# Kernel optimization log

Measured on AMD Instinct MI355X. Metric: run time of the kernel, lower is better.

The kernel has to match this reference:

```python
import jax, jax.numpy as jnp
import numpy as np

EPS = 1e-5
N_GROUP = 1

def _linear(x, w, b):
    # w: [in, out], b: [out]
    return x @ w + b

def _group_norm_per_sample(x, weight, bias, n_group=N_GROUP, eps=EPS):
    # x: [B, C]; weight/bias: [B, C] (per-sample hypernet-generated affine).
    # F.group_norm on 2D input normalizes each sample over its channel groups.
    B, C = x.shape
    xr = x.reshape(B, n_group, C // n_group)
    m = jnp.mean(xr, axis=-1, keepdims=True)
    v = jnp.mean((xr - m) ** 2, axis=-1, keepdims=True)
    xn = ((xr - m) * jax.lax.rsqrt(v + eps)).reshape(B, C)
    return xn * weight + bias

def setup_inputs() -> dict:
    key = jax.random.key(0)
    ks = jax.random.split(key, 32)
    B, P, CIN, COUT = 32768, 8, 512, 256
    s = 0.05
    d = {}
    d['x_feature'] = jax.random.normal(ks[0], (B, CIN), dtype=jnp.float32)
    d['x_param'] = jax.random.normal(ks[1], (B, P), dtype=jnp.float32)
    # hypernet for norm1 weight/bias (P -> 32 -> 2048)
    d['hw1_1_w'] = jax.random.normal(ks[2], (P, 32)) * s;   d['hw1_1_b'] = jnp.zeros((32,))
    d['hw1_2_w'] = jax.random.normal(ks[3], (32, 2048)) * s; d['hw1_2_b'] = jnp.ones((2048,))
    d['hb1_1_w'] = jax.random.normal(ks[4], (P, 32)) * s;   d['hb1_1_b'] = jnp.zeros((32,))
    d['hb1_2_w'] = jax.random.normal(ks[5], (32, 2048)) * s; d['hb1_2_b'] = jnp.zeros((2048,))
    # hypernet for norm2 weight/bias (P -> 32 -> 1024)
    d['hw2_1_w'] = jax.random.normal(ks[6], (P, 32)) * s;   d['hw2_1_b'] = jnp.zeros((32,))
    d['hw2_2_w'] = jax.random.normal(ks[7], (32, 1024)) * s; d['hw2_2_b'] = jnp.ones((1024,))
    d['hb2_1_w'] = jax.random.normal(ks[8], (P, 32)) * s;   d['hb2_1_b'] = jnp.zeros((32,))
    d['hb2_2_w'] = jax.random.normal(ks[9], (32, 1024)) * s; d['hb2_2_b'] = jnp.zeros((1024,))
    # base net
    d['l1_w'] = jax.random.normal(ks[10], (CIN, 2048)) * s;  d['l1_b'] = jnp.zeros((2048,))
    d['l2_w'] = jax.random.normal(ks[11], (2048, 1024)) * s; d['l2_b'] = jnp.zeros((1024,))
    d['l3_w'] = jax.random.normal(ks[12], (1024, COUT)) * s; d['l3_b'] = jnp.zeros((COUT,))
    return d

def reference(x_feature, x_param,
              hw1_1_w, hw1_1_b, hw1_2_w, hw1_2_b,
              hb1_1_w, hb1_1_b, hb1_2_w, hb1_2_b,
              hw2_1_w, hw2_1_b, hw2_2_w, hw2_2_b,
              hb2_1_w, hb2_1_b, hb2_2_w, hb2_2_b,
              l1_w, l1_b, l2_w, l2_b, l3_w, l3_b):
    # hypernet: per-sample group-norm affine params
    p = x_param  # already n_level columns
    w1 = _linear(jax.nn.relu(_linear(p, hw1_1_w, hw1_1_b)), hw1_2_w, hw1_2_b)  # [B, 2048]
    b1 = _linear(jax.nn.relu(_linear(p, hb1_1_w, hb1_1_b)), hb1_2_w, hb1_2_b)  # [B, 2048]
    w2 = _linear(jax.nn.relu(_linear(p, hw2_1_w, hw2_1_b)), hw2_2_w, hw2_2_b)  # [B, 1024]
    b2 = _linear(jax.nn.relu(_linear(p, hb2_1_w, hb2_1_b)), hb2_2_w, hb2_2_b)  # [B, 1024]
    # base net with per-sample affine group norm (vectorized form of the torch
    # host-side grouping loop: samples with identical x_param share identical
    # generated affine params, and group_norm stats are per-sample anyway)
    x = _linear(x_feature, l1_w, l1_b)            # [B, 2048]
    x = jax.nn.relu(_group_norm_per_sample(x, w1, b1))
    x = _linear(x, l2_w, l2_b)                    # [B, 1024]
    x = jax.nn.relu(_group_norm_per_sample(x, w2, b2))
    x = _linear(x, l3_w, l3_b)                    # [B, 256]
    return jax.nn.log_softmax(x, axis=1)
```

## Files before the change

kernel.cpp:

```cpp
#include <hip/hip_runtime.h>

typedef unsigned short u16;
typedef float f32x4 __attribute__((ext_vector_type(4)));
typedef __bf16 bf16x8 __attribute__((ext_vector_type(8)));
typedef u16 u16x4 __attribute__((ext_vector_type(4)));
typedef u16 u16x8 __attribute__((ext_vector_type(8)));

__device__ __forceinline__ float bf2f(u16 u) {
    unsigned int x = ((unsigned int)u) << 16;
    return __builtin_bit_cast(float, x);
}
__device__ __forceinline__ u16 f2bf(float f) {
    unsigned int x = __builtin_bit_cast(unsigned int, f);
    x += 0x7fffu + ((x >> 16) & 1u);
    return (u16)(x >> 16);
}

#define GLD16(gp, lp)                                                          \
    __builtin_amdgcn_global_load_lds(                                          \
        (const __attribute__((address_space(1))) void*)(gp),                   \
        (__attribute__((address_space(3))) void*)(lp), 16, 0, 0)

__global__ void f32_to_bf16_k(const float* __restrict__ in, u16* __restrict__ out, long n4) {
    long i = (long)blockIdx.x * 256 + threadIdx.x;
    if (i >= n4) return;
    f32x4 v = *reinterpret_cast<const f32x4*>(in + i * 4);
    u16x4 o;
    o[0] = f2bf(v[0]); o[1] = f2bf(v[1]); o[2] = f2bf(v[2]); o[3] = f2bf(v[3]);
    *reinterpret_cast<u16x4*>(out + i * 4) = o;
}

__global__ void transpose_f32_bf16(const float* __restrict__ in, u16* __restrict__ out,
                                   int R, int C) {
    __shared__ float tile[32][33];
    const int bx = blockIdx.x * 32;
    const int by = blockIdx.y * 32;
    const int tx = threadIdx.x;
    const int ty0 = threadIdx.y;
    #pragma unroll
    for (int ty = ty0; ty < 32; ty += 8)
        tile[ty][tx] = in[(long)(by + ty) * C + bx + tx];
    __syncthreads();
    #pragma unroll
    for (int ty = ty0; ty < 32; ty += 8)
        out[(long)(bx + ty) * R + by + tx] = f2bf(tile[tx][ty]);
}

__global__ void hyper_h(const float* __restrict__ P, const float* __restrict__ W,
                        const float* __restrict__ b, u16* __restrict__ H, int B_) {
    const int idx = blockIdx.x * 256 + threadIdx.x;
    const int s = idx >> 5, c = idx & 31;
    if (s >= B_) return;
    float acc = b[c];
    #pragma unroll
    for (int k = 0; k < 8; ++k) acc += P[s * 8 + k] * W[k * 32 + c];
    H[idx] = f2bf(fmaxf(acc, 0.f));
}

template <int OUT_BF16>
__global__ __launch_bounds__(256, 2) void gemm_bt(
    const u16* __restrict__ A, const u16* __restrict__ BT,
    const float* __restrict__ bias, u16* __restrict__ Cb, float* __restrict__ Cf,
    int M, int N, int K) {
    __shared__ __align__(16) u16 As[128 * 64];
    __shared__ __align__(16) u16 Bs[128 * 64];
    const int tid = threadIdx.x;
    const int lane = tid & 63;
    const int wave = tid >> 6;
    const int wr = wave >> 1, wc = wave & 1;
    const long row0 = (long)blockIdx.x * 128;
    const long col0 = (long)blockIdx.y * 128;

    const int srow = tid >> 3;
    const int scol = (tid & 7) * 8;
    const u16* Ag = A + (row0 + srow) * (long)K + scol;
    const u16* Bg = BT + (col0 + srow) * (long)K + scol;
    u16* AsW = As + (size_t)(wave * 64) * 8;
    u16* BsW = Bs + (size_t)(wave * 64) * 8;

    f32x4 acc[4][4] = {};

    for (int k0 = 0; k0 < K; k0 += 64) {
        #pragma unroll
        for (int i = 0; i < 4; ++i) {
            GLD16(Ag + (long)i * 32 * K + k0, AsW + i * 256 * 8);
            GLD16(Bg + (long)i * 32 * K + k0, BsW + i * 256 * 8);
        }
        __syncthreads();
        #pragma unroll
        for (int kk = 0; kk < 2; ++kk) {
            bf16x8 af[4], bfr[4];
            #pragma unroll
            for (int m = 0; m < 4; ++m)
                af[m] = *reinterpret_cast<const bf16x8*>(
                    As + (wr * 64 + m * 16 + (lane & 15)) * 64 + kk * 32 + (lane >> 4) * 8);
            #pragma unroll
            for (int n = 0; n < 4; ++n)
                bfr[n] = *reinterpret_cast<const bf16x8*>(
                    Bs + (wc * 64 + n * 16 + (lane & 15)) * 64 + kk * 32 + (lane >> 4) * 8);
            #pragma unroll
            for (int m = 0; m < 4; ++m)
                #pragma unroll
                for (int n = 0; n < 4; ++n)
                    acc[m][n] = __builtin_amdgcn_mfma_f32_16x16x32_bf16(af[m], bfr[n],
                                                                        acc[m][n], 0, 0, 0);
        }
        __syncthreads();
    }

    #pragma unroll
    for (int n = 0; n < 4; ++n) {
        const long col = col0 + wc * 64 + n * 16 + (lane & 15);
        const float bv = bias[col];
        #pragma unroll
        for (int m = 0; m < 4; ++m) {
            const long rowb = row0 + wr * 64 + m * 16 + ((lane >> 4) * 4);
            #pragma unroll
            for (int r = 0; r < 4; ++r) {
                const float v = acc[m][n][r] + bv;
                if (OUT_BF16) Cb[(rowb + r) * (long)N + col] = f2bf(v);
                else          Cf[(rowb + r) * (long)N + col] = v;
            }
        }
    }
}

template <int C>
__global__ __launch_bounds__(256, 2) void gn_affine(
    u16* __restrict__ Y,
    const u16* __restrict__ Hw, const u16* __restrict__ Hb,
    const u16* __restrict__ WwT, const u16* __restrict__ WbT,
    const float* __restrict__ bw, const float* __restrict__ bb) {
    const int tid = threadIdx.x;
    const int lane = tid & 63;
    const int wave = tid >> 6;
    const long r0 = (long)blockIdx.x * 32;
    __shared__ float mean_l[32], rs_l[32];
    __shared__ __align__(16) float wt[32][132];
    __shared__ __align__(16) float btl[32][132];

    const int row = tid >> 3, sub = tid & 7;

    {
        float s = 0.f, ss = 0.f;
        const u16* yr = Y + (r0 + row) * (long)C;
        for (int c = sub * 16; c < C; c += 128) {
            u16x8 v0 = *reinterpret_cast<const u16x8*>(yr + c);
            u16x8 v1 = *reinterpret_cast<const u16x8*>(yr + c + 8);
            #pragma unroll
            for (int j = 0; j < 8; ++j) {
                float f0 = bf2f(v0[j]), f1 = bf2f(v1[j]);
                s += f0 + f1;
                ss += f0 * f0 + f1 * f1;
            }
        }
        s  += __shfl_xor(s, 1);  s  += __shfl_xor(s, 2);  s  += __shfl_xor(s, 4);
        ss += __shfl_xor(ss, 1); ss += __shfl_xor(ss, 2); ss += __shfl_xor(ss, 4);
        if (sub == 0) {
            float m = s / (float)C;
            float var = fmaxf(ss / (float)C - m * m, 0.f);
            mean_l[row] = m;
            rs_l[row] = rsqrtf(var + 1e-5f);
        }
    }
    __syncthreads();

    const int mm = wave & 1;
    const int npair = wave >> 1;
    const bf16x8 ha = *reinterpret_cast<const bf16x8*>(
        Hw + (r0 + mm * 16 + (lane & 15)) * 32 + (lane >> 4) * 8);
    const bf16x8 hbf = *reinterpret_cast<const bf16x8*>(
        Hb + (r0 + mm * 16 + (lane & 15)) * 32 + (lane >> 4) * 8);

    for (int c0 = 0; c0 < C; c0 += 128) {
        #pragma unroll
        for (int j = 0; j < 4; ++j) {
            const int n = npair * 4 + j;
            const int cl = c0 + n * 16 + (lane & 15);
            const bf16x8 wv = *reinterpret_cast<const bf16x8*>(WwT + (long)cl * 32 + (lane >> 4) * 8);
            const bf16x8 bv = *reinterpret_cast<const bf16x8*>(WbT + (long)cl * 32 + (lane >> 4) * 8);
            f32x4 z = {0.f, 0.f, 0.f, 0.f};
            f32x4 wa = __builtin_amdgcn_mfma_f32_16x16x32_bf16(ha, wv, z, 0, 0, 0);
            f32x4 ba = __builtin_amdgcn_mfma_f32_16x16x32_bf16(hbf, bv, z, 0, 0, 0);
            const float bwv = bw[cl], bbv = bb[cl];
            const int ncol = n * 16 + (lane & 15);
            #pragma unroll
            for (int r = 0; r < 4; ++r) {
                const int rl = mm * 16 + (lane >> 4) * 4 + r;
                wt[rl][ncol]  = wa[r] + bwv;
                btl[rl][ncol] = ba[r] + bbv;
            }
        }
        __syncthreads();
        {
            const long base = (r0 + row) * (long)C + c0 + sub * 16;
            u16x8 v0 = *reinterpret_cast<const u16x8*>(Y + base);
            u16x8 v1 = *reinterpret_cast<const u16x8*>(Y + base + 8);
            const float mu = mean_l[row], rs = rs_l[row];
            u16x8 o0, o1;
            #pragma unroll
            for (int j = 0; j < 8; ++j) {
                float f = (bf2f(v0[j]) - mu) * rs;
                f = f * wt[row][sub * 16 + j] + btl[row][sub * 16 + j];
                o0[j] = f2bf(fmaxf(f, 0.f));
                float g = (bf2f(v1[j]) - mu) * rs;
                g = g * wt[row][sub * 16 + 8 + j] + btl[row][sub * 16 + 8 + j];
                o1[j] = f2bf(fmaxf(g, 0.f));
            }
            *reinterpret_cast<u16x8*>(Y + base) = o0;
            *reinterpret_cast<u16x8*>(Y + base + 8) = o1;
        }
        __syncthreads();
    }
}

__global__ __launch_bounds__(256) void logsoftmax256(const float* __restrict__ X,
                                                     float* __restrict__ O) {
    const int wave = threadIdx.x >> 6, lane = threadIdx.x & 63;
    const long row = (long)blockIdx.x * 4 + wave;
    const float* x = X + row * 256 + lane * 4;
    f32x4 v = *reinterpret_cast<const f32x4*>(x);
    float mx = fmaxf(fmaxf(v[0], v[1]), fmaxf(v[2], v[3]));
    #pragma unroll
    for (int d = 1; d < 64; d <<= 1) mx = fmaxf(mx, __shfl_xor(mx, d));
    float s = 0.f;
    #pragma unroll
    for (int j = 0; j < 4; ++j) s += __expf(v[j] - mx);
    #pragma unroll
    for (int d = 1; d < 64; d <<= 1) s += __shfl_xor(s, d);
    const float lse = mx + logf(s);
    f32x4 o;
    #pragma unroll
    for (int j = 0; j < 4; ++j) o[j] = v[j] - lse;
    *reinterpret_cast<f32x4*>(O + row * 256 + lane * 4) = o;
}

extern "C" void kernel_launch(void* const* d_in, const int* in_sizes, int n_in,
                              void* d_out, int out_size, void* d_ws, size_t ws_size,
                              hipStream_t stream) {
    const float* x_feature = (const float*)d_in[0];
    const float* x_param   = (const float*)d_in[1];
    const float* hw1_1_w = (const float*)d_in[2];
    const float* hw1_1_b = (const float*)d_in[3];
    const float* hw1_2_w = (const float*)d_in[4];
    const float* hw1_2_b = (const float*)d_in[5];
    const float* hb1_1_w = (const float*)d_in[6];
    const float* hb1_1_b = (const float*)d_in[7];
    const float* hb1_2_w = (const float*)d_in[8];
    const float* hb1_2_b = (const float*)d_in[9];
    const float* hw2_1_w = (const float*)d_in[10];
    const float* hw2_1_b = (const float*)d_in[11];
    const float* hw2_2_w = (const float*)d_in[12];
    const float* hw2_2_b = (const float*)d_in[13];
    const float* hb2_1_w = (const float*)d_in[14];
    const float* hb2_1_b = (const float*)d_in[15];
    const float* hb2_2_w = (const float*)d_in[16];
    const float* hb2_2_b = (const float*)d_in[17];
    const float* l1_w = (const float*)d_in[18];
    const float* l1_b = (const float*)d_in[19];
    const float* l2_w = (const float*)d_in[20];
    const float* l2_b = (const float*)d_in[21];
    const float* l3_w = (const float*)d_in[22];
    const float* l3_b = (const float*)d_in[23];

    const int B = in_sizes[0] / 512;
    constexpr int CIN = 512, C1 = 2048, C2 = 1024, COUT = 256;

    char* p = (char*)d_ws;
    auto carve = [&](size_t bytes) {
        char* q = p;
        p += (bytes + 255) & ~(size_t)255;
        return q;
    };
    u16* xb    = (u16*)carve((size_t)B * CIN * 2);
    u16* y1    = (u16*)carve((size_t)B * C1 * 2);
    u16* y2    = (u16*)carve((size_t)B * C2 * 2);
    u16* w1T   = (u16*)carve((size_t)C1 * CIN * 2);
    u16* w2T   = (u16*)carve((size_t)C2 * C1 * 2);
    u16* w3T   = (u16*)carve((size_t)COUT * C2 * 2);
    u16* hw12T = (u16*)carve((size_t)C1 * 32 * 2);
    u16* hb12T = (u16*)carve((size_t)C1 * 32 * 2);
    u16* hw22T = (u16*)carve((size_t)C2 * 32 * 2);
    u16* hb22T = (u16*)carve((size_t)C2 * 32 * 2);
    u16* Hw1   = (u16*)carve((size_t)B * 32 * 2);
    u16* Hb1   = (u16*)carve((size_t)B * 32 * 2);
    u16* Hw2   = (u16*)carve((size_t)B * 32 * 2);
    u16* Hb2   = (u16*)carve((size_t)B * 32 * 2);
    float* logits = (float*)y1;

    f32_to_bf16_k<<<(B * CIN / 4 + 255) / 256, 256, 0, stream>>>(x_feature, xb, (long)B * CIN / 4);
    dim3 tb(32, 8);
    transpose_f32_bf16<<<dim3(C1 / 32, CIN / 32), tb, 0, stream>>>(l1_w, w1T, CIN, C1);
    transpose_f32_bf16<<<dim3(C2 / 32, C1 / 32), tb, 0, stream>>>(l2_w, w2T, C1, C2);
    transpose_f32_bf16<<<dim3(COUT / 32, C2 / 32), tb, 0, stream>>>(l3_w, w3T, C2, COUT);
    transpose_f32_bf16<<<dim3(C1 / 32, 1), tb, 0, stream>>>(hw1_2_w, hw12T, 32, C1);
    transpose_f32_bf16<<<dim3(C1 / 32, 1), tb, 0, stream>>>(hb1_2_w, hb12T, 32, C1);
    transpose_f32_bf16<<<dim3(C2 / 32, 1), tb, 0, stream>>>(hw2_2_w, hw22T, 32, C2);
    transpose_f32_bf16<<<dim3(C2 / 32, 1), tb, 0, stream>>>(hb2_2_w, hb22T, 32, C2);
    hyper_h<<<B * 32 / 256, 256, 0, stream>>>(x_param, hw1_1_w, hw1_1_b, Hw1, B);
    hyper_h<<<B * 32 / 256, 256, 0, stream>>>(x_param, hb1_1_w, hb1_1_b, Hb1, B);
    hyper_h<<<B * 32 / 256, 256, 0, stream>>>(x_param, hw2_1_w, hw2_1_b, Hw2, B);
    hyper_h<<<B * 32 / 256, 256, 0, stream>>>(x_param, hb2_1_w, hb2_1_b, Hb2, B);

    gemm_bt<1><<<dim3(B / 128, C1 / 128), 256, 0, stream>>>(xb, w1T, l1_b, y1, nullptr, B, C1, CIN);
    gn_affine<C1><<<B / 32, 256, 0, stream>>>(y1, Hw1, Hb1, hw12T, hb12T, hw1_2_b, hb1_2_b);
    gemm_bt<1><<<dim3(B / 128, C2 / 128), 256, 0, stream>>>(y1, w2T, l2_b, y2, nullptr, B, C2, C1);
    gn_affine<C2><<<B / 32, 256, 0, stream>>>(y2, Hw2, Hb2, hw22T, hb22T, hw2_2_b, hb2_2_b);
    gemm_bt<0><<<dim3(B / 128, COUT / 128), 256, 0, stream>>>(y2, w3T, l3_b, nullptr, logits, B, COUT, C2);
    logsoftmax256<<<B / 4, 256, 0, stream>>>(logits, (float*)d_out);
}
```

Before: 640.8 us.

## Add 256x256 pipelined GEMM with fused row stats, merge hypernet kernels

Replaces the 128x128 GEMM for the first two layers with a 512-thread 256x256 tile kernel. It double-buffers LDS through global_load_lds, uses XOR-swizzled LDS addressing, a block-index swizzle and s_setprio around the MFMAs. That GEMM also writes per-row partial sum and sum-of-squares, so the group-norm kernel no longer re-reads the activation to compute statistics. The four hypernet first-layer launches are merged into one kernel. In exchange, statistics come from fp32 values before bf16 rounding, and the large tile relies on K being a multiple of 128.

```diff
diff --git a/kernel.cpp b/kernel.cpp
--- a/kernel.cpp
+++ b/kernel.cpp
@@ -46,15 +46,230 @@
         out[(long)(bx + ty) * R + by + tx] = f2bf(tile[tx][ty]);
 }
 
-__global__ void hyper_h(const float* __restrict__ P, const float* __restrict__ W,
-                        const float* __restrict__ b, u16* __restrict__ H, int B_) {
+__global__ void hyper_h4(const float* __restrict__ P,
+                         const float* __restrict__ Wa, const float* __restrict__ ba, u16* __restrict__ Ha,
+                         const float* __restrict__ Wb, const float* __restrict__ bb_, u16* __restrict__ Hb,
+                         const float* __restrict__ Wc, const float* __restrict__ bc, u16* __restrict__ Hc,
+                         const float* __restrict__ Wd, const float* __restrict__ bd, u16* __restrict__ Hd,
+                         int B_) {
     const int idx = blockIdx.x * 256 + threadIdx.x;
+    if (idx >= B_ * 32) return;
     const int s = idx >> 5, c = idx & 31;
-    if (s >= B_) return;
-    float acc = b[c];
-    #pragma unroll
-    for (int k = 0; k < 8; ++k) acc += P[s * 8 + k] * W[k * 32 + c];
-    H[idx] = f2bf(fmaxf(acc, 0.f));
+    float p[8];
+    #pragma unroll
+    for (int k = 0; k < 8; ++k) p[k] = P[s * 8 + k];
+    auto one = [&](const float* W, const float* b, u16* H) {
+        float a = b[c];
+        #pragma unroll
+        for (int k = 0; k < 8; ++k) a += p[k] * W[k * 32 + c];
+        H[idx] = f2bf(fmaxf(a, 0.f));
+    };
+    one(Wa, ba, Ha); one(Wb, bb_, Hb); one(Wc, bc, Hc); one(Wd, bd, Hd);
+}
+
+template <int OUT_BF16, int STATS>
+__global__ __launch_bounds__(512, 2) void gemm256(
+    const u16* __restrict__ A, const u16* __restrict__ BT,
+    const float* __restrict__ bias, u16* __restrict__ Cb, float* __restrict__ Cf,
+    float* __restrict__ stats, int M, int N, int K, int mblocks) {
+    __shared__ __align__(16) u16 lds[2][2][2][128 * 64];
+    const int tid = threadIdx.x;
+    const int lane = tid & 63;
+    const int wave = tid >> 6;
+    const int wr = wave & 1;
+    const int wc = wave >> 1;
+
+    const int nwg = gridDim.x;
+    const int bid = blockIdx.x;
+    const int swz = (bid & 7) * (nwg >> 3) + (bid >> 3);
+    const int bx = swz % mblocks;
+    const int by = swz / mblocks;
+    const long row0 = (long)bx * 256;
+    const long col0 = (long)by * 256;
+
+    const int srow = tid >> 3;
+    const int scb = ((tid & 7) * 16) ^ (((tid >> 5) & 1) << 5);
+    const long sAoff = (row0 + srow) * (long)K + (scb >> 1);
+    const long sBoff = (col0 + srow) * (long)K + (scb >> 1);
+
+    auto STAGE = [&](int buf, int ab, int half, int kt) {
+        const u16* g = (ab ? BT : A) + (ab ? sBoff : sAoff) + (long)half * 128 * K + (long)kt * 64;
+        u16* d = &lds[buf][ab][half][tid * 8];
+        GLD16(g, d);
+        GLD16(g + 64 * (long)K, d + 4096);
+    };
+
+    const int ln15 = lane & 15, ln16 = lane >> 4;
+    const int swz_b = ((ln15 >> 2) & 1) << 5;
+    const int cbe0 = ((ln16 * 16) ^ swz_b) >> 1;
+    const int arow = (wr * 64 + ln15) * 64;
+    const int brow = (wc * 32 + ln15) * 64;
+
+    f32x4 acc[8][4] = {};
+
+#define PHASE(BUF, AH, BH, SAB, SH, KT)                                          \
+    {                                                                            \
+        asm volatile("s_waitcnt vmcnt(4)" ::: "memory");                         \
+        __builtin_amdgcn_sched_barrier(0);                                       \
+        __builtin_amdgcn_s_barrier();                                            \
+        __builtin_amdgcn_sched_barrier(0);                                       \
+        STAGE((BUF) ^ 1, SAB, SH, KT);                                           \
+        bf16x8 aF[4][2], bF[2][2];                                               \
+        const u16* ap = &lds[BUF][0][AH][0];                                     \
+        const u16* bp = &lds[BUF][1][BH][0];                                     \
+        _Pragma("unroll") for (int ml = 0; ml < 4; ++ml)                         \
+            _Pragma("unroll") for (int kk = 0; kk < 2; ++kk)                     \
+                aF[ml][kk] = *(const bf16x8*)(ap + arow + ml * 1024 + cbe0 + kk * 32); \
+        _Pragma("unroll") for (int nl = 0; nl < 2; ++nl)                         \
+            _Pragma("unroll") for (int kk = 0; kk < 2; ++kk)                     \
+                bF[nl][kk] = *(const bf16x8*)(bp + brow + nl * 1024 + cbe0 + kk * 32); \
+        __builtin_amdgcn_s_setprio(1);                                           \
+        _Pragma("unroll") for (int ml = 0; ml < 4; ++ml)                         \
+            _Pragma("unroll") for (int nl = 0; nl < 2; ++nl)                     \
+                _Pragma("unroll") for (int kk = 0; kk < 2; ++kk)                 \
+                    acc[(AH) * 4 + ml][(BH) * 2 + nl] =                          \
+                        __builtin_amdgcn_mfma_f32_16x16x32_bf16(                 \
+                            aF[ml][kk], bF[nl][kk], acc[(AH) * 4 + ml][(BH) * 2 + nl], 0, 0, 0); \
+        __builtin_amdgcn_s_setprio(0);                                           \
+    }
+
+    STAGE(0, 0, 0, 0); STAGE(0, 1, 0, 0); STAGE(0, 0, 1, 0); STAGE(0, 1, 1, 0);
+
+    const int nt = K >> 6;
+    for (int it = 0; it < (nt >> 1); ++it) {
+        const int t0 = it * 2;
+        const int ka = t0 + 1;
+        const int kb = (t0 + 2 < nt) ? t0 + 2 : nt - 1;
+        PHASE(0, 0, 0, 0, 0, ka)
+        PHASE(0, 1, 0, 1, 0, ka)
+        PHASE(0, 1, 1, 0, 1, ka)
+        PHASE(0, 0, 1, 1, 1, ka)
+        PHASE(1, 0, 0, 0, 0, kb)
+        PHASE(1, 1, 0, 1, 0, kb)
+        PHASE(1, 1, 1, 0, 1, kb)
+        PHASE(1, 0, 1, 1, 1, kb)
+    }
+#undef PHASE
+    asm volatile("s_waitcnt vmcnt(0)" ::: "memory");
+
+    float bv[4];
+    #pragma unroll
+    for (int n = 0; n < 4; ++n)
+        bv[n] = bias[col0 + wc * 32 + (n & 1) * 16 + (n >> 1) * 128 + ln15];
+
+    #pragma unroll
+    for (int m = 0; m < 8; ++m) {
+        const long rowb = row0 + wr * 64 + (m & 3) * 16 + (m >> 2) * 128 + ln16 * 4;
+        #pragma unroll
+        for (int n = 0; n < 4; ++n) {
+            const long col = col0 + wc * 32 + (n & 1) * 16 + (n >> 1) * 128 + ln15;
+            #pragma unroll
+            for (int r = 0; r < 4; ++r) {
+                const float v = acc[m][n][r] + bv[n];
+                if (OUT_BF16) Cb[(rowb + r) * (long)N + col] = f2bf(v);
+                else          Cf[(rowb + r) * (long)N + col] = v;
+            }
+        }
+        if (STATS) {
+            #pragma unroll
+            for (int r = 0; r < 4; ++r) {
+                float s = 0.f, ss = 0.f;
+                #pragma unroll
+                for (int n = 0; n < 4; ++n) {
+                    const float v = acc[m][n][r] + bv[n];
+                    s += v; ss += v * v;
+                }
+                #pragma unroll
+                for (int d = 1; d < 16; d <<= 1) { s += __shfl_xor(s, d); ss += __shfl_xor(ss, d); }
+                if (ln15 == 0) {
+                    float* sp = stats + (((long)by * 4 + wc) * M + rowb + r) * 2;
+                    sp[0] = s; sp[1] = ss;
+                }
+            }
+        }
+    }
+}
+
+template <int C, int NPART>
+__global__ __launch_bounds__(256, 2) void gn_affine(
+    u16* __restrict__ Y, const float* __restrict__ stats, int Btot,
+    const u16* __restrict__ Hw, const u16* __restrict__ Hb,
+    const u16* __restrict__ WwT, const u16* __restrict__ WbT,
+    const float* __restrict__ bw, const float* __restrict__ bb) {
+    const int tid = threadIdx.x;
+    const int lane = tid & 63;
+    const int wave = tid >> 6;
+    const long r0 = (long)blockIdx.x * 32;
+    __shared__ float mean_l[32], rs_l[32];
+    __shared__ __align__(16) float wt[32][132];
+    __shared__ __align__(16) float btl[32][132];
+
+    const int row = tid >> 3, sub = tid & 7;
+
+    {
+        float s = 0.f, ss = 0.f;
+        for (int p_ = sub; p_ < NPART; p_ += 8) {
+            const float* sp = stats + ((long)p_ * Btot + (r0 + row)) * 2;
+            s += sp[0]; ss += sp[1];
+        }
+        s  += __shfl_xor(s, 1);  s  += __shfl_xor(s, 2);  s  += __shfl_xor(s, 4);
+        ss += __shfl_xor(ss, 1); ss += __shfl_xor(ss, 2); ss += __shfl_xor(ss, 4);
+        if (sub == 0) {
+            float m = s / (float)C;
+            float var = fmaxf(ss / (float)C - m * m, 0.f);
+            mean_l[row] = m;
+            rs_l[row] = rsqrtf(var + 1e-5f);
+        }
+    }
+    __syncthreads();
+
+    const int mm = wave & 1;
+    const int npair = wave >> 1;
+    const bf16x8 ha = *reinterpret_cast<const bf16x8*>(
+        Hw + (r0 + mm * 16 + (lane & 15)) * 32 + (lane >> 4) * 8);
+    const bf16x8 hbf = *reinterpret_cast<const bf16x8*>(
+        Hb + (r0 + mm * 16 + (lane & 15)) * 32 + (lane >> 4) * 8);
+
+    for (int c0 = 0; c0 < C; c0 += 128) {
+        #pragma unroll
+        for (int j = 0; j < 4; ++j) {
+            const int n = npair * 4 + j;
+            const int cl = c0 + n * 16 + (lane & 15);
+            const bf16x8 wv = *reinterpret_cast<const bf16x8*>(WwT + (long)cl * 32 + (lane >> 4) * 8);
+            const bf16x8 bv = *reinterpret_cast<const bf16x8*>(WbT + (long)cl * 32 + (lane >> 4) * 8);
+            f32x4 z = {0.f, 0.f, 0.f, 0.f};
+            f32x4 wa = __builtin_amdgcn_mfma_f32_16x16x32_bf16(ha, wv, z, 0, 0, 0);
+            f32x4 ba = __builtin_amdgcn_mfma_f32_16x16x32_bf16(hbf, bv, z, 0, 0, 0);
+            const float bwv = bw[cl], bbv = bb[cl];
+            const int ncol = n * 16 + (lane & 15);
+            #pragma unroll
+            for (int r = 0; r < 4; ++r) {
+                const int rl = mm * 16 + (lane >> 4) * 4 + r;
+                wt[rl][ncol]  = wa[r] + bwv;
+                btl[rl][ncol] = ba[r] + bbv;
+            }
+        }
+        __syncthreads();
+        {
+            const long base = (r0 + row) * (long)C + c0 + sub * 16;
+            u16x8 v0 = *reinterpret_cast<const u16x8*>(Y + base);
+            u16x8 v1 = *reinterpret_cast<const u16x8*>(Y + base + 8);
+            const float mu = mean_l[row], rs = rs_l[row];
+            u16x8 o0, o1;
+            #pragma unroll
+            for (int j = 0; j < 8; ++j) {
+                float f = (bf2f(v0[j]) - mu) * rs;
+                f = f * wt[row][sub * 16 + j] + btl[row][sub * 16 + j];
+                o0[j] = f2bf(fmaxf(f, 0.f));
+                float g = (bf2f(v1[j]) - mu) * rs;
+                g = g * wt[row][sub * 16 + 8 + j] + btl[row][sub * 16 + 8 + j];
+                o1[j] = f2bf(fmaxf(g, 0.f));
+            }
+            *reinterpret_cast<u16x8*>(Y + base) = o0;
+            *reinterpret_cast<u16x8*>(Y + base + 8) = o1;
+        }
+        __syncthreads();
+    }
 }
 
 template <int OUT_BF16>
@@ -111,106 +326,17 @@
     #pragma unroll
     for (int n = 0; n < 4; ++n) {
         const long col = col0 + wc * 64 + n * 16 + (lane & 15);
-        const float bv = bias[col];
+        const float bvv = bias[col];
         #pragma unroll
         for (int m = 0; m < 4; ++m) {
             const long rowb = row0 + wr * 64 + m * 16 + ((lane >> 4) * 4);
             #pragma unroll
             for (int r = 0; r < 4; ++r) {
-                const float v = acc[m][n][r] + bv;
+                const float v = acc[m][n][r] + bvv;
                 if (OUT_BF16) Cb[(rowb + r) * (long)N + col] = f2bf(v);
                 else          Cf[(rowb + r) * (long)N + col] = v;
             }
         }
-    }
-}
-
-template <int C>
-__global__ __launch_bounds__(256, 2) void gn_affine(
-    u16* __restrict__ Y,
-    const u16* __restrict__ Hw, const u16* __restrict__ Hb,
-    const u16* __restrict__ WwT, const u16* __restrict__ WbT,
-    const float* __restrict__ bw, const float* __restrict__ bb) {
-    const int tid = threadIdx.x;
-    const int lane = tid & 63;
-    const int wave = tid >> 6;
-    const long r0 = (long)blockIdx.x * 32;
-    __shared__ float mean_l[32], rs_l[32];
-    __shared__ __align__(16) float wt[32][132];
-    __shared__ __align__(16) float btl[32][132];
-
-    const int row = tid >> 3, sub = tid & 7;
-
-    {
-        float s = 0.f, ss = 0.f;
-        const u16* yr = Y + (r0 + row) * (long)C;
-        for (int c = sub * 16; c < C; c += 128) {
-            u16x8 v0 = *reinterpret_cast<const u16x8*>(yr + c);
-            u16x8 v1 = *reinterpret_cast<const u16x8*>(yr + c + 8);
-            #pragma unroll
-            for (int j = 0; j < 8; ++j) {
-                float f0 = bf2f(v0[j]), f1 = bf2f(v1[j]);
-                s += f0 + f1;
-                ss += f0 * f0 + f1 * f1;
-            }
-        }
-        s  += __shfl_xor(s, 1);  s  += __shfl_xor(s, 2);  s  += __shfl_xor(s, 4);
-        ss += __shfl_xor(ss, 1); ss += __shfl_xor(ss, 2); ss += __shfl_xor(ss, 4);
-        if (sub == 0) {
-            float m = s / (float)C;
-            float var = fmaxf(ss / (float)C - m * m, 0.f);
-            mean_l[row] = m;
-            rs_l[row] = rsqrtf(var + 1e-5f);
-        }
-    }
-    __syncthreads();
-
-    const int mm = wave & 1;
-    const int npair = wave >> 1;
-    const bf16x8 ha = *reinterpret_cast<const bf16x8*>(
-        Hw + (r0 + mm * 16 + (lane & 15)) * 32 + (lane >> 4) * 8);
-    const bf16x8 hbf = *reinterpret_cast<const bf16x8*>(
-        Hb + (r0 + mm * 16 + (lane & 15)) * 32 + (lane >> 4) * 8);
-
-    for (int c0 = 0; c0 < C; c0 += 128) {
-        #pragma unroll
-        for (int j = 0; j < 4; ++j) {
-            const int n = npair * 4 + j;
-            const int cl = c0 + n * 16 + (lane & 15);
-            const bf16x8 wv = *reinterpret_cast<const bf16x8*>(WwT + (long)cl * 32 + (lane >> 4) * 8);
-            const bf16x8 bv = *reinterpret_cast<const bf16x8*>(WbT + (long)cl * 32 + (lane >> 4) * 8);
-            f32x4 z = {0.f, 0.f, 0.f, 0.f};
-            f32x4 wa = __builtin_amdgcn_mfma_f32_16x16x32_bf16(ha, wv, z, 0, 0, 0);
-            f32x4 ba = __builtin_amdgcn_mfma_f32_16x16x32_bf16(hbf, bv, z, 0, 0, 0);
-            const float bwv = bw[cl], bbv = bb[cl];
-            const int ncol = n * 16 + (lane & 15);
-            #pragma unroll
-            for (int r = 0; r < 4; ++r) {
-                const int rl = mm * 16 + (lane >> 4) * 4 + r;
-                wt[rl][ncol]  = wa[r] + bwv;
-                btl[rl][ncol] = ba[r] + bbv;
-            }
-        }
-        __syncthreads();
-        {
-            const long base = (r0 + row) * (long)C + c0 + sub * 16;
-            u16x8 v0 = *reinterpret_cast<const u16x8*>(Y + base);
-            u16x8 v1 = *reinterpret_cast<const u16x8*>(Y + base + 8);
-            const float mu = mean_l[row], rs = rs_l[row];
-            u16x8 o0, o1;
-            #pragma unroll
-            for (int j = 0; j < 8; ++j) {
-                float f = (bf2f(v0[j]) - mu) * rs;
-                f = f * wt[row][sub * 16 + j] + btl[row][sub * 16 + j];
-                o0[j] = f2bf(fmaxf(f, 0.f));
-                float g = (bf2f(v1[j]) - mu) * rs;
-                g = g * wt[row][sub * 16 + 8 + j] + btl[row][sub * 16 + 8 + j];
-                o1[j] = f2bf(fmaxf(g, 0.f));
-            }
-            *reinterpret_cast<u16x8*>(Y + base) = o0;
-            *reinterpret_cast<u16x8*>(Y + base + 8) = o1;
-        }
-        __syncthreads();
     }
 }
 
@@ -286,6 +412,8 @@
     u16* Hb1   = (u16*)carve((size_t)B * 32 * 2);
     u16* Hw2   = (u16*)carve((size_t)B * 32 * 2);
     u16* Hb2   = (u16*)carve((size_t)B * 32 * 2);
+    float* stat1 = (float*)carve((size_t)(C1 / 256) * 4 * B * 2 * 4);
+    float* stat2 = (float*)carve((size_t)(C2 / 256) * 4 * B * 2 * 4);
     float* logits = (float*)y1;
 
     f32_to_bf16_k<<<(B * CIN / 4 + 255) / 256, 256, 0, stream>>>(x_feature, xb, (long)B * CIN / 4);
@@ -297,15 +425,19 @@
     transpose_f32_bf16<<<dim3(C1 / 32, 1), tb, 0, stream>>>(hb1_2_w, hb12T, 32, C1);
     transpose_f32_bf16<<<dim3(C2 / 32, 1), tb, 0, stream>>>(hw2_2_w, hw22T, 32, C2);
     transpose_f32_bf16<<<dim3(C2 / 32, 1), tb, 0, stream>>>(hb2_2_w, hb22T, 32, C2);
-    hyper_h<<<B * 32 / 256, 256, 0, stream>>>(x_param, hw1_1_w, hw1_1_b, Hw1, B);
-    hyper_h<<<B * 32 / 256, 256, 0, stream>>>(x_param, hb1_1_w, hb1_1_b, Hb1, B);
-    hyper_h<<<B * 32 / 256, 256, 0, stream>>>(x_param, hw2_1_w, hw2_1_b, Hw2, B);
-    hyper_h<<<B * 32 / 256, 256, 0, stream>>>(x_param, hb2_1_w, hb2_1_b, Hb2, B);
-
-    gemm_bt<1><<<dim3(B / 128, C1 / 128), 256, 0, stream>>>(xb, w1T, l1_b, y1, nullptr, B, C1, CIN);
-    gn_affine<C1><<<B / 32, 256, 0, stream>>>(y1, Hw1, Hb1, hw12T, hb12T, hw1_2_b, hb1_2_b);
-    gemm_bt<1><<<dim3(B / 128, C2 / 128), 256, 0, stream>>>(y1, w2T, l2_b, y2, nullptr, B, C2, C1);
-    gn_affine<C2><<<B / 32, 256, 0, stream>>>(y2, Hw2, Hb2, hw22T, hb22T, hw2_2_b, hb2_2_b);
-    gemm_bt<0><<<dim3(B / 128, COUT / 128), 256, 0, stream>>>(y2, w3T, l3_b, nullptr, logits, B, COUT, C2);
+    hyper_h4<<<B * 32 / 256, 256, 0, stream>>>(x_param,
+        hw1_1_w, hw1_1_b, Hw1, hb1_1_w, hb1_1_b, Hb1,
+        hw2_1_w, hw2_1_b, Hw2, hb2_1_w, hb2_1_b, Hb2, B);
+
+    gemm256<1, 1><<<(B / 256) * (C1 / 256), 512, 0, stream>>>(
+        xb, w1T, l1_b, y1, nullptr, stat1, B, C1, CIN, B / 256);
+    gn_affine<C1, (C1 / 256) * 4><<<B / 32, 256, 0, stream>>>(
+        y1, stat1, B, Hw1, Hb1, hw12T, hb12T, hw1_2_b, hb1_2_b);
+    gemm256<1, 1><<<(B / 256) * (C2 / 256), 512, 0, stream>>>(
+        y1, w2T, l2_b, y2, nullptr, stat2, B, C2, C1, B / 256);
+    gn_affine<C2, (C2 / 256) * 4><<<B / 32, 256, 0, stream>>>(
+        y2, stat2, B, Hw2, Hb2, hw22T, hb22T, hw2_2_b, hb2_2_b);
+    gemm_bt<0><<<dim3(B / 128, COUT / 128), 256, 0, stream>>>(
+        y2, w3T, l3_b, nullptr, logits, B, COUT, C2);
     logsoftmax256<<<B / 4, 256, 0, stream>>>(logits, (float*)d_out);
 }
```

Measured after the change: 599.6 us. 1.07x faster.
